# Kernel optimization log

Measured on AMD Instinct MI355X. Metric: run time of the kernel, lower is better.

## Reference

```python
import jax, jax.numpy as jnp
import numpy as np
import math

EMBED_DIM = 1024
MEMORY_DIM = 1024
MEMORY_SIZE = 2048
B, S = 8, 4096


def bitnet_linear(x, W, b):
    """Eval-mode BitNetLinear: 1.58-bit weight quant + 8-bit activation quant."""
    w_scale = jnp.mean(jnp.abs(W))
    qW = jnp.sign(W) * (jnp.abs(W) > 0.5 * w_scale).astype(W.dtype)
    i_scale = jnp.max(jnp.abs(x)) / 127.0
    qx = jnp.clip(jnp.round(x / i_scale), -128.0, 127.0)
    out = jnp.einsum('bsi,oi->bso', qx, qW) * (w_scale * i_scale)
    return out + b


def setup_inputs() -> dict:
    key = jax.random.key(0)
    ks = jax.random.split(key, 9)
    return {
        'x': jax.random.normal(ks[0], (B, S, EMBED_DIM), jnp.float32),
        'memory_keys': jax.random.normal(ks[1], (MEMORY_SIZE, MEMORY_DIM), jnp.float32),
        'memory_values': jax.random.normal(ks[2], (MEMORY_SIZE, EMBED_DIM), jnp.float32),
        'Wk': jax.random.normal(ks[3], (MEMORY_DIM, EMBED_DIM), jnp.float32) * 0.1,
        'bk': jnp.zeros((MEMORY_DIM,), jnp.float32),
        'Wv': jax.random.normal(ks[4], (EMBED_DIM, EMBED_DIM), jnp.float32) * 0.1,
        'bv': jnp.zeros((EMBED_DIM,), jnp.float32),
        'Wo': jax.random.normal(ks[5], (EMBED_DIM, EMBED_DIM), jnp.float32) * 0.1,
        'bo': jnp.zeros((EMBED_DIM,), jnp.float32),
    }


def reference(x, memory_keys, memory_values, Wk, bk, Wv, bv, Wo, bo):
    # quantized key/value projections
    query_keys = bitnet_linear(x, Wk, bk)          # [B, S, Dm]
    _query_values = bitnet_linear(x, Wv, bv)       # computed in original (used only by update path)
    # memory cross-attention over fixed bank
    similarities = jnp.einsum('bsd,md->bsm', query_keys, memory_keys)  # [B, S, M]
    attention_weights = jax.nn.softmax(similarities / math.sqrt(MEMORY_DIM), axis=-1)
    retrieved = jnp.einsum('bsm,me->bse', attention_weights, memory_values)  # [B, S, E]
    output = bitnet_linear(x + retrieved, Wo, bo)
    return output
```

## Files before the change

kernel.cpp:

```cpp
#include <hip/hip_runtime.h>
#include <hip/hip_bf16.h>
#include <stdint.h>
#include <type_traits>

typedef __attribute__((ext_vector_type(8))) short bf16x8;
typedef __attribute__((ext_vector_type(4))) float f32x4;
typedef __attribute__((ext_vector_type(4))) int i32x4;

struct Scalars {
  double sum_wk;
  double sum_wo;
  unsigned int max_x_bits;
  unsigned int max_y_bits;
};

__device__ __forceinline__ unsigned short f2bf(float f) {
  __hip_bfloat16 h = __float2bfloat16(f);
  return *reinterpret_cast<unsigned short*>(&h);
}

__device__ __forceinline__ void async16(void* lds, const void* g) {
  __builtin_amdgcn_global_load_lds((__attribute__((address_space(1))) void*)g,
                                   (__attribute__((address_space(3))) void*)lds, 16, 0, 0);
}

__device__ __forceinline__ void tile_swizzle(int nxShift, int& bx, int& by) {
  const int per = gridDim.x >> 3;
  const int tile = (blockIdx.x & 7) * per + (blockIdx.x >> 3);
  bx = tile & ((1 << nxShift) - 1);
  by = tile >> nxShift;
}

__device__ __forceinline__ f32x4 mm(bf16x8 a, bf16x8 b, f32x4 c) {
  return __builtin_amdgcn_mfma_f32_16x16x32_bf16(a, b, c, 0, 0, 0);
}
__device__ __forceinline__ i32x4 mm(i32x4 a, i32x4 b, i32x4 c) {
  return __builtin_amdgcn_mfma_i32_16x16x64_i8(a, b, c, 0, 0, 0);
}

__global__ __launch_bounds__(256) void abssum_kernel(const float* __restrict__ w, size_t n,
                                                     double* __restrict__ out) {
  size_t tid = (size_t)blockIdx.x * blockDim.x + threadIdx.x;
  size_t stride = (size_t)gridDim.x * blockDim.x;
  double s = 0.0;
  for (size_t i = tid * 4; i < n; i += stride * 4) {
    float4 v = *(const float4*)(w + i);
    s += (double)fabsf(v.x) + (double)fabsf(v.y) + (double)fabsf(v.z) + (double)fabsf(v.w);
  }
#pragma unroll
  for (int o = 32; o > 0; o >>= 1) s += __shfl_xor(s, o);
  __shared__ double sm[4];
  if ((threadIdx.x & 63) == 0) sm[threadIdx.x >> 6] = s;
  __syncthreads();
  if (threadIdx.x == 0) atomicAdd(out, sm[0] + sm[1] + sm[2] + sm[3]);
}

__global__ __launch_bounds__(256) void absmax_kernel(const float* __restrict__ x, size_t n,
                                                     unsigned int* __restrict__ out) {
  size_t tid = (size_t)blockIdx.x * blockDim.x + threadIdx.x;
  size_t stride = (size_t)gridDim.x * blockDim.x;
  float m = 0.0f;
  for (size_t i = tid * 4; i < n; i += stride * 4) {
    float4 v = *(const float4*)(x + i);
    m = fmaxf(m, fmaxf(fmaxf(fabsf(v.x), fabsf(v.y)), fmaxf(fabsf(v.z), fabsf(v.w))));
  }
#pragma unroll
  for (int o = 32; o > 0; o >>= 1) m = fmaxf(m, __shfl_xor(m, o));
  __shared__ float sm[4];
  if ((threadIdx.x & 63) == 0) sm[threadIdx.x >> 6] = m;
  __syncthreads();
  if (threadIdx.x == 0)
    atomicMax(out, __float_as_uint(fmaxf(fmaxf(sm[0], sm[1]), fmaxf(sm[2], sm[3]))));
}

__global__ __launch_bounds__(256) void quant_act_i8_kernel(const float* __restrict__ x,
                                                           char* __restrict__ q,
                                                           const unsigned int* __restrict__ maxbits,
                                                           size_t n) {
  const float isc = __uint_as_float(*maxbits) / 127.0f;
  size_t tid = (size_t)blockIdx.x * blockDim.x + threadIdx.x;
  size_t stride = (size_t)gridDim.x * blockDim.x;
  for (size_t i = tid * 4; i < n; i += stride * 4) {
    float4 v = *(const float4*)(x + i);
    char4 o;
    o.x = (char)(int)fminf(fmaxf(rintf(v.x / isc), -128.f), 127.f);
    o.y = (char)(int)fminf(fmaxf(rintf(v.y / isc), -128.f), 127.f);
    o.z = (char)(int)fminf(fmaxf(rintf(v.z / isc), -128.f), 127.f);
    o.w = (char)(int)fminf(fmaxf(rintf(v.w / isc), -128.f), 127.f);
    *(char4*)(q + i) = o;
  }
}

__global__ __launch_bounds__(256) void quant_w_i8_kernel(const float* __restrict__ W,
                                                         char* __restrict__ qW,
                                                         const double* __restrict__ sum, size_t n) {
  const float wsc = (float)(*sum / (double)n);
  const float thr = 0.5f * wsc;
  size_t tid = (size_t)blockIdx.x * blockDim.x + threadIdx.x;
  size_t stride = (size_t)gridDim.x * blockDim.x;
  for (size_t i = tid * 4; i < n; i += stride * 4) {
    float4 v = *(const float4*)(W + i);
    char4 o;
    o.x = (char)(fabsf(v.x) > thr ? (v.x > 0.f ? 1 : -1) : 0);
    o.y = (char)(fabsf(v.y) > thr ? (v.y > 0.f ? 1 : -1) : 0);
    o.z = (char)(fabsf(v.z) > thr ? (v.z > 0.f ? 1 : -1) : 0);
    o.w = (char)(fabsf(v.w) > thr ? (v.w > 0.f ? 1 : -1) : 0);
    *(char4*)(qW + i) = o;
  }
}

__global__ __launch_bounds__(256) void cast_bf16_kernel(const float* __restrict__ src,
                                                        __hip_bfloat16* __restrict__ dst,
                                                        size_t n) {
  size_t tid = (size_t)blockIdx.x * blockDim.x + threadIdx.x;
  size_t stride = (size_t)gridDim.x * blockDim.x;
  for (size_t i = tid * 4; i < n; i += stride * 4) {
    float4 v = *(const float4*)(src + i);
    ushort4 o;
    o.x = f2bf(v.x); o.y = f2bf(v.y); o.z = f2bf(v.z); o.w = f2bf(v.w);
    *(ushort4*)((unsigned short*)dst + i) = o;
  }
}

__global__ void transpose_mv_kernel(const float* __restrict__ mv,
                                    __hip_bfloat16* __restrict__ mvT) {
  __shared__ float tile[32][33];
  int tx = threadIdx.x, ty = threadIdx.y;
  int e = blockIdx.x * 32 + tx;
  int m = blockIdx.y * 32 + ty;
  tile[ty][tx] = mv[(size_t)m * 1024 + e];
  __syncthreads();
  int om = blockIdx.y * 32 + tx;
  mvT[(size_t)(blockIdx.x * 32 + ty) * 2048 + om] = __float2bfloat16(tile[tx][ty]);
}

__global__ __launch_bounds__(256) void softmax_kernel(__hip_bfloat16* __restrict__ sims) {
  unsigned short* row = (unsigned short*)(sims + (size_t)blockIdx.x * 2048);
  const int t = threadIdx.x;
  const int l = t & 63, wv = t >> 6;
  uint4 r4 = *(const uint4*)(row + t * 8);
  float v[8];
  v[0] = __uint_as_float(r4.x << 16); v[1] = __uint_as_float(r4.x & 0xffff0000u);
  v[2] = __uint_as_float(r4.y << 16); v[3] = __uint_as_float(r4.y & 0xffff0000u);
  v[4] = __uint_as_float(r4.z << 16); v[5] = __uint_as_float(r4.z & 0xffff0000u);
  v[6] = __uint_as_float(r4.w << 16); v[7] = __uint_as_float(r4.w & 0xffff0000u);
  float m = v[0];
#pragma unroll
  for (int i = 1; i < 8; ++i) m = fmaxf(m, v[i]);
#pragma unroll
  for (int o = 32; o > 0; o >>= 1) m = fmaxf(m, __shfl_xor(m, o));
  __shared__ float red[4], red2[4];
  if (l == 0) red[wv] = m;
  __syncthreads();
  m = fmaxf(fmaxf(red[0], red[1]), fmaxf(red[2], red[3]));
  float s = 0.f;
#pragma unroll
  for (int i = 0; i < 8; ++i) { v[i] = expf(v[i] - m); s += v[i]; }
#pragma unroll
  for (int o = 32; o > 0; o >>= 1) s += __shfl_xor(s, o);
  if (l == 0) red2[wv] = s;
  __syncthreads();
  s = red2[0] + red2[1] + red2[2] + red2[3];
  unsigned short b[8];
#pragma unroll
  for (int i = 0; i < 8; ++i) b[i] = f2bf(v[i] / s);
  uint4 o4;
  o4.x = (unsigned)b[0] | ((unsigned)b[1] << 16);
  o4.y = (unsigned)b[2] | ((unsigned)b[3] << 16);
  o4.z = (unsigned)b[4] | ((unsigned)b[5] << 16);
  o4.w = (unsigned)b[6] | ((unsigned)b[7] << 16);
  *(uint4*)(row + t * 8) = o4;
}

#define CFENCE() asm volatile("" ::: "memory")
#define BAR8() { CFENCE(); __builtin_amdgcn_s_barrier(); CFENCE(); }
#define WLGKM(N) { asm volatile("s_waitcnt lgkmcnt(" #N ")" ::: "memory"); __builtin_amdgcn_sched_barrier(0); }
#define WVM(N) asm volatile("s_waitcnt vmcnt(" #N ")" ::: "memory")

template <int EPI>
__global__ __launch_bounds__(512, 2) void gemm8(
    const char* __restrict__ A, const char* __restrict__ B, void* __restrict__ C,
    const float* __restrict__ aux, Scalars* __restrict__ sc,
    int Ndim, int KB, int nxShift) {
  constexpr bool I8 = (EPI >= 3);
  using FR  = typename std::conditional<I8, i32x4, bf16x8>::type;
  using ACC = typename std::conditional<I8, i32x4, f32x4>::type;
  __shared__ __align__(16) char lds[4][2][16384];

  int bx, by;
  tile_swizzle(nxShift, bx, by);
  const int rowBlk = by * 256, colBlk = bx * 256;

  const int t = threadIdx.x, w = t >> 6, l = t & 63;
  const int wm = w >> 2, wn = w & 3;
  const int quad = l >> 4, m16 = l & 15;
  const int NT = KB >> 7, NIT = NT >> 1;

  int voA[2][2], voB[2][2];
#pragma unroll
  for (int hf = 0; hf < 2; ++hf)
#pragma unroll
    for (int j = 0; j < 2; ++j) {
      const int idx = j * 64 + (t >> 3);
      const int kby = ((t & 7) ^ (idx & 7)) << 4;
      voA[hf][j] = (rowBlk + ((idx >> 6) << 7) + (hf << 6) + (idx & 63)) * KB + kby;
      voB[hf][j] = (colBlk + ((idx >> 5) << 6) + (hf << 5) + (idx & 31)) * KB + kby;
    }

  const char* baA[2];
  const char* baB[2];
#pragma unroll
  for (int ks = 0; ks < 2; ++ks) {
    const int x16 = ((ks << 6) + (quad << 4)) ^ ((m16 & 7) << 4);
    baA[ks] = &lds[0][0][(wm * 64 + m16) * 128 + x16];
    baB[ks] = &lds[2][0][(wn * 32 + m16) * 128 + x16];
  }

#define STG_A(slot, hf, tk)                                                         \
  if ((tk) < NT) {                                                                  \
    _Pragma("unroll") for (int j = 0; j < 2; ++j)                                   \
      async16(&lds[hf][slot][j * 8192 + (w << 10)],                                 \
              A + (((size_t)(tk)) << 7) + voA[hf][j]);                              \
  }
#define STG_B(slot, hf, tk)                                                         \
  if ((tk) < NT) {                                                                  \
    _Pragma("unroll") for (int j = 0; j < 2; ++j)                                   \
      async16(&lds[2 + (hf)][slot][j * 8192 + (w << 10)],                           \
              B + (((size_t)(tk)) << 7) + voB[hf][j]);                              \
  }

#define LD_A(dst, slot, hf, f, ks) \
  dst = *(const FR*)(baA[ks] + ((hf)*32768 + (slot)*16384 + (f)*2048));
#define LD_B(dst, slot, hf, gg, ks) \
  dst = *(const FR*)(baB[ks] + ((hf)*32768 + (slot)*16384 + (gg)*2048));

#define R_A0(s) { _Pragma("unroll") for (int f_ = 0; f_ < 4; ++f_) { LD_A(af[f_][0], s, 0, f_, 0); LD_A(af[f_][1], s, 0, f_, 1); } }
#define R_A1(s) { _Pragma("unroll") for (int f_ = 0; f_ < 4; ++f_) { LD_A(af[f_][0], s, 1, f_, 0); LD_A(af[f_][1], s, 1, f_, 1); } }
#define R_B0(s) { _Pragma("unroll") for (int g_ = 0; g_ < 2; ++g_) { LD_B(b0[g_][0], s, 0, g_, 0); LD_B(b0[g_][1], s, 0, g_, 1); } }
#define R_B1(s) { _Pragma("unroll") for (int g_ = 0; g_ < 2; ++g_) { LD_B(b1[g_][0], s, 1, g_, 0); LD_B(b1[g_][1], s, 1, g_, 1); } }

#define MM8(FO, GO, BR)                                                             \
  __builtin_amdgcn_s_setprio(1);                                                    \
  _Pragma("unroll") for (int f_ = 0; f_ < 4; ++f_)                                  \
    _Pragma("unroll") for (int g_ = 0; g_ < 2; ++g_) {                              \
      acc[(FO) + f_][(GO) + g_] = mm(af[f_][0], BR[g_][0], acc[(FO) + f_][(GO) + g_]); \
      acc[(FO) + f_][(GO) + g_] = mm(af[f_][1], BR[g_][1], acc[(FO) + f_][(GO) + g_]); \
    }                                                                               \
  __builtin_amdgcn_s_setprio(0);

#define TSTEP(s, tk, last)                                                          \
  {                                                                                 \
                     \
    R_B1(s);                                                                        \
    STG_A((s) ^ 1, 1, (tk) + 1);                                                    \
    BAR8(); WLGKM(4);                                                               \
    MM8(0, 0, b0);                                                                  \
    BAR8();                                                                         \
        \
    STG_A(s, 0, (tk) + 2);                                                          \
    BAR8(); WLGKM(0);                                                               \
    MM8(0, 2, b1);                                                                  \
    R_A1(s);                                                                        \
    BAR8();                                                                         \
                                                                \
    STG_B(s, 0, (tk) + 2);                                                          \
    BAR8(); WLGKM(0);                                                               \
    MM8(4, 0, b0);                                                                  \
    BAR8();                                                                         \
           \
    STG_B(s, 1, (tk) + 2);                                                          \
    if (last) { WVM(0); } else { WVM(6); }                                          \
    BAR8();                                                                         \
    MM8(4, 2, b1);                                                                  \
    R_A0((s) ^ 1);                                                                  \
    R_B0((s) ^ 1);                                                                  \
    BAR8();                                                                         \
  }

  FR af[4][2], b0[2][2], b1[2][2];
  ACC acc[8][4] = {};

  STG_A(0, 0, 0); STG_B(0, 0, 0); STG_B(0, 1, 0); STG_A(0, 1, 0);
  CFENCE();
  STG_A(1, 0, 1); STG_B(1, 0, 1); STG_B(1, 1, 1);
  WVM(6);
  BAR8();
  R_A0(0); R_B0(0);

  for (int it = 0; it < NIT; ++it) {
    const bool last = (it == NIT - 1);
    TSTEP(0, it * 2, last);
    TSTEP(1, it * 2 + 1, last);
  }

  float sK = 0.0f;
  if constexpr (EPI == 3)
    sK = (float)(sc->sum_wk * (1.0 / 1048576.0)) * (__uint_as_float(sc->max_x_bits) / 127.0f);
  if constexpr (EPI == 4)
    sK = (float)(sc->sum_wo * (1.0 / 1048576.0)) * (__uint_as_float(sc->max_y_bits) / 127.0f);

  float amax = 0.0f;
#pragma unroll
  for (int f = 0; f < 8; ++f) {
#pragma unroll
    for (int g = 0; g < 4; ++g) {
      const int col = colBlk + wn * 64 + g * 16 + m16;
#pragma unroll
      for (int rg = 0; rg < 4; ++rg) {
        const int row = rowBlk + wm * 128 + f * 16 + quad * 4 + rg;
        if constexpr (EPI == 1) {
          ((__hip_bfloat16*)C)[(size_t)row * Ndim + col] =
              __float2bfloat16(acc[f][g][rg] * 0.03125f);
        } else if constexpr (EPI == 2) {
          float v = acc[f][g][rg] + aux[(size_t)row * Ndim + col];
          ((float*)C)[(size_t)row * Ndim + col] = v;
          amax = fmaxf(amax, fabsf(v));
        } else if constexpr (EPI == 3) {
          ((__hip_bfloat16*)C)[(size_t)row * Ndim + col] =
              __float2bfloat16((float)acc[f][g][rg] * sK + aux[col]);
        } else {
          ((float*)C)[(size_t)row * Ndim + col] = (float)acc[f][g][rg] * sK + aux[col];
        }
      }
    }
  }

  if constexpr (EPI == 2) {
    __shared__ float wred[8];
#pragma unroll
    for (int o = 32; o > 0; o >>= 1) amax = fmaxf(amax, __shfl_xor(amax, o));
    if (l == 0) wred[w] = amax;
    __syncthreads();
    if (t == 0) {
      float m = wred[0];
#pragma unroll
      for (int i = 1; i < 8; ++i) m = fmaxf(m, wred[i]);
      atomicMax(&sc->max_y_bits, __float_as_uint(m));
    }
  }
#undef STG_A
#undef STG_B
#undef LD_A
#undef LD_B
#undef R_A0
#undef R_A1
#undef R_B0
#undef R_B1
#undef MM8
#undef TSTEP
}

extern "C" void kernel_launch(void* const* d_in, const int* in_sizes, int n_in,
                              void* d_out, int out_size, void* d_ws, size_t ws_size,
                              hipStream_t stream) {
  (void)in_sizes; (void)n_in; (void)out_size; (void)ws_size;
  const float* x  = (const float*)d_in[0];
  const float* mk = (const float*)d_in[1];
  const float* mv = (const float*)d_in[2];
  const float* Wk = (const float*)d_in[3];
  const float* bk = (const float*)d_in[4];
  const float* Wo = (const float*)d_in[7];
  const float* bo = (const float*)d_in[8];
  float* out = (float*)d_out;

  const int M = 32768, E = 1024, MEM = 2048;

  char* ws = (char*)d_ws;
  Scalars* sc = (Scalars*)ws;
  const size_t off0 = 256;
  char* qx8 = ws + off0;
  __hip_bfloat16* qk = (__hip_bfloat16*)(ws + off0 + (size_t)M * E);
  float* y = (float*)(ws + off0);
  const size_t off1 = off0 + (size_t)M * E * 4;
  __hip_bfloat16* sims = (__hip_bfloat16*)(ws + off1);
  char* qy8 = (char*)sims;
  const size_t off2 = off1 + (size_t)M * MEM * 2;
  char* qWk8 = ws + off2;
  char* qWo8 = qWk8 + (size_t)E * E;
  __hip_bfloat16* mkb = (__hip_bfloat16*)(qWo8 + (size_t)E * E);
  __hip_bfloat16* mvT = mkb + (size_t)MEM * E;

  hipMemsetAsync(ws, 0, 256, stream);

  abssum_kernel<<<dim3(256), dim3(256), 0, stream>>>(Wk, (size_t)E * E, &sc->sum_wk);
  abssum_kernel<<<dim3(256), dim3(256), 0, stream>>>(Wo, (size_t)E * E, &sc->sum_wo);
  absmax_kernel<<<dim3(2048), dim3(256), 0, stream>>>(x, (size_t)M * E, &sc->max_x_bits);

  quant_act_i8_kernel<<<dim3(2048), dim3(256), 0, stream>>>(x, qx8, &sc->max_x_bits, (size_t)M * E);
  quant_w_i8_kernel<<<dim3(256), dim3(256), 0, stream>>>(Wk, qWk8, &sc->sum_wk, (size_t)E * E);
  quant_w_i8_kernel<<<dim3(256), dim3(256), 0, stream>>>(Wo, qWo8, &sc->sum_wo, (size_t)E * E);
  cast_bf16_kernel<<<dim3(256), dim3(256), 0, stream>>>(mk, mkb, (size_t)MEM * E);
  transpose_mv_kernel<<<dim3(E / 32, MEM / 32), dim3(32, 32), 0, stream>>>(mv, mvT);

  gemm8<3><<<dim3((E / 256) * (M / 256)), dim3(512), 0, stream>>>(
      qx8, qWk8, qk, bk, sc, E, E, 2);
  gemm8<1><<<dim3((MEM / 256) * (M / 256)), dim3(512), 0, stream>>>(
      (const char*)qk, (const char*)mkb, sims, nullptr, sc, MEM, 2 * E, 3);
  softmax_kernel<<<dim3(M), dim3(256), 0, stream>>>(sims);
  gemm8<2><<<dim3((E / 256) * (M / 256)), dim3(512), 0, stream>>>(
      (const char*)sims, (const char*)mvT, y, x, sc, E, 2 * MEM, 2);
  quant_act_i8_kernel<<<dim3(2048), dim3(256), 0, stream>>>(y, qy8, &sc->max_y_bits, (size_t)M * E);
  gemm8<4><<<dim3((E / 256) * (M / 256)), dim3(512), 0, stream>>>(
      qy8, qWo8, out, bo, sc, E, E, 2);
}
```

Before: 774.4 us.

## Switch GEMMs to 32x32 MFMA and merge prep kernels into two launches

Replaces the 16x16 MFMA tiles in the templated GEMM with 32x32x16 bf16 and 32x32x32 i8 MFMAs, which changes the LDS fragment addressing, swizzle offsets and epilogue row mapping. It also fuses the abssum and absmax reductions into one stats kernel and the weight quantisation, bf16 cast, transpose and activation quantisation into one prep kernel. The aim is fewer LDS reads per MFMA, higher matrix throughput and less launch overhead. The trailing barrier in the pipeline step is removed, which risks LDS races, and the new lane mapping risks correctness errors.

```diff
diff --git a/kernel.cpp b/kernel.cpp
--- a/kernel.cpp
+++ b/kernel.cpp
@@ -4,8 +4,9 @@
 #include <type_traits>
 
 typedef __attribute__((ext_vector_type(8))) short bf16x8;
-typedef __attribute__((ext_vector_type(4))) float f32x4;
 typedef __attribute__((ext_vector_type(4))) int i32x4;
+typedef __attribute__((ext_vector_type(16))) float f32x16;
+typedef __attribute__((ext_vector_type(16))) int i32x16;
 
 struct Scalars {
   double sum_wk;
@@ -31,46 +32,112 @@
   by = tile >> nxShift;
 }
 
-__device__ __forceinline__ f32x4 mm(bf16x8 a, bf16x8 b, f32x4 c) {
-  return __builtin_amdgcn_mfma_f32_16x16x32_bf16(a, b, c, 0, 0, 0);
-}
-__device__ __forceinline__ i32x4 mm(i32x4 a, i32x4 b, i32x4 c) {
-  return __builtin_amdgcn_mfma_i32_16x16x64_i8(a, b, c, 0, 0, 0);
-}
-
-__global__ __launch_bounds__(256) void abssum_kernel(const float* __restrict__ w, size_t n,
-                                                     double* __restrict__ out) {
-  size_t tid = (size_t)blockIdx.x * blockDim.x + threadIdx.x;
-  size_t stride = (size_t)gridDim.x * blockDim.x;
-  double s = 0.0;
-  for (size_t i = tid * 4; i < n; i += stride * 4) {
-    float4 v = *(const float4*)(w + i);
-    s += (double)fabsf(v.x) + (double)fabsf(v.y) + (double)fabsf(v.z) + (double)fabsf(v.w);
-  }
-#pragma unroll
-  for (int o = 32; o > 0; o >>= 1) s += __shfl_xor(s, o);
-  __shared__ double sm[4];
-  if ((threadIdx.x & 63) == 0) sm[threadIdx.x >> 6] = s;
-  __syncthreads();
-  if (threadIdx.x == 0) atomicAdd(out, sm[0] + sm[1] + sm[2] + sm[3]);
-}
-
-__global__ __launch_bounds__(256) void absmax_kernel(const float* __restrict__ x, size_t n,
-                                                     unsigned int* __restrict__ out) {
-  size_t tid = (size_t)blockIdx.x * blockDim.x + threadIdx.x;
-  size_t stride = (size_t)gridDim.x * blockDim.x;
-  float m = 0.0f;
-  for (size_t i = tid * 4; i < n; i += stride * 4) {
-    float4 v = *(const float4*)(x + i);
-    m = fmaxf(m, fmaxf(fmaxf(fabsf(v.x), fabsf(v.y)), fmaxf(fabsf(v.z), fabsf(v.w))));
-  }
-#pragma unroll
-  for (int o = 32; o > 0; o >>= 1) m = fmaxf(m, __shfl_xor(m, o));
-  __shared__ float sm[4];
-  if ((threadIdx.x & 63) == 0) sm[threadIdx.x >> 6] = m;
-  __syncthreads();
-  if (threadIdx.x == 0)
-    atomicMax(out, __float_as_uint(fmaxf(fmaxf(sm[0], sm[1]), fmaxf(sm[2], sm[3]))));
+__device__ __forceinline__ f32x16 mm32(bf16x8 a, bf16x8 b, f32x16 c) {
+  return __builtin_amdgcn_mfma_f32_32x32x16_bf16(a, b, c, 0, 0, 0);
+}
+__device__ __forceinline__ i32x16 mm32(i32x4 a, i32x4 b, i32x16 c) {
+  return __builtin_amdgcn_mfma_i32_32x32x32_i8(a, b, c, 0, 0, 0);
+}
+
+__global__ __launch_bounds__(256) void stats_kernel(const float* __restrict__ Wk,
+                                                    const float* __restrict__ Wo,
+                                                    const float* __restrict__ x,
+                                                    Scalars* __restrict__ sc) {
+  const int which = blockIdx.y;
+  size_t tid = (size_t)blockIdx.x * 256 + threadIdx.x;
+  size_t stride = (size_t)gridDim.x * 256;
+  if (which < 2) {
+    const float* w = which ? Wo : Wk;
+    const size_t n = 1048576;
+    double s = 0.0;
+    for (size_t i = tid * 4; i < n; i += stride * 4) {
+      float4 v = *(const float4*)(w + i);
+      s += (double)fabsf(v.x) + (double)fabsf(v.y) + (double)fabsf(v.z) + (double)fabsf(v.w);
+    }
+#pragma unroll
+    for (int o = 32; o > 0; o >>= 1) s += __shfl_xor(s, o);
+    __shared__ double sm[4];
+    if ((threadIdx.x & 63) == 0) sm[threadIdx.x >> 6] = s;
+    __syncthreads();
+    if (threadIdx.x == 0)
+      atomicAdd(which ? &sc->sum_wo : &sc->sum_wk, sm[0] + sm[1] + sm[2] + sm[3]);
+  } else {
+    const size_t n = (size_t)32768 * 1024;
+    float m = 0.0f;
+    for (size_t i = tid * 4; i < n; i += stride * 4) {
+      float4 v = *(const float4*)(x + i);
+      m = fmaxf(m, fmaxf(fmaxf(fabsf(v.x), fabsf(v.y)), fmaxf(fabsf(v.z), fabsf(v.w))));
+    }
+#pragma unroll
+    for (int o = 32; o > 0; o >>= 1) m = fmaxf(m, __shfl_xor(m, o));
+    __shared__ float smf[4];
+    if ((threadIdx.x & 63) == 0) smf[threadIdx.x >> 6] = m;
+    __syncthreads();
+    if (threadIdx.x == 0)
+      atomicMax(&sc->max_x_bits,
+                __float_as_uint(fmaxf(fmaxf(smf[0], smf[1]), fmaxf(smf[2], smf[3]))));
+  }
+}
+
+__global__ __launch_bounds__(256) void prep_kernel(
+    const float* __restrict__ Wk, const float* __restrict__ Wo,
+    const float* __restrict__ mk, const float* __restrict__ mv,
+    const float* __restrict__ x, char* __restrict__ qWk8, char* __restrict__ qWo8,
+    __hip_bfloat16* __restrict__ mkb, __hip_bfloat16* __restrict__ mvT,
+    char* __restrict__ qx8, const Scalars* __restrict__ sc) {
+  __shared__ float tl[32][33];
+  const int which = blockIdx.y;
+  const int t = threadIdx.x;
+  size_t tid = (size_t)blockIdx.x * 256 + t;
+  size_t stride = (size_t)gridDim.x * 256;
+  if (which < 2) {
+    const float* W = which ? Wo : Wk;
+    char* q = which ? qWo8 : qWk8;
+    const double sum = which ? sc->sum_wo : sc->sum_wk;
+    const float thr = 0.5f * (float)(sum * (1.0 / 1048576.0));
+    const size_t n = 1048576;
+    for (size_t i = tid * 4; i < n; i += stride * 4) {
+      float4 v = *(const float4*)(W + i);
+      char4 o;
+      o.x = (char)(fabsf(v.x) > thr ? (v.x > 0.f ? 1 : -1) : 0);
+      o.y = (char)(fabsf(v.y) > thr ? (v.y > 0.f ? 1 : -1) : 0);
+      o.z = (char)(fabsf(v.z) > thr ? (v.z > 0.f ? 1 : -1) : 0);
+      o.w = (char)(fabsf(v.w) > thr ? (v.w > 0.f ? 1 : -1) : 0);
+      *(char4*)(q + i) = o;
+    }
+  } else if (which == 2) {
+    const size_t n = (size_t)2048 * 1024;
+    for (size_t i = tid * 4; i < n; i += stride * 4) {
+      float4 v = *(const float4*)(mk + i);
+      ushort4 o;
+      o.x = f2bf(v.x); o.y = f2bf(v.y); o.z = f2bf(v.z); o.w = f2bf(v.w);
+      *(ushort4*)((unsigned short*)mkb + i) = o;
+    }
+  } else if (which == 3) {
+    const int ti = blockIdx.x & 31;
+    const int tj = blockIdx.x >> 5;
+    const int tx = t & 31, ty = t >> 5;
+#pragma unroll
+    for (int r = 0; r < 4; ++r)
+      tl[ty + r * 8][tx] = mv[(size_t)(tj * 32 + ty + r * 8) * 1024 + ti * 32 + tx];
+    __syncthreads();
+#pragma unroll
+    for (int r = 0; r < 4; ++r)
+      mvT[(size_t)(ti * 32 + ty + r * 8) * 2048 + tj * 32 + tx] =
+          __float2bfloat16(tl[tx][ty + r * 8]);
+  } else {
+    const float isc = __uint_as_float(sc->max_x_bits) / 127.0f;
+    const size_t n = (size_t)32768 * 1024;
+    for (size_t i = tid * 4; i < n; i += stride * 4) {
+      float4 v = *(const float4*)(x + i);
+      char4 o;
+      o.x = (char)(int)fminf(fmaxf(rintf(v.x / isc), -128.f), 127.f);
+      o.y = (char)(int)fminf(fmaxf(rintf(v.y / isc), -128.f), 127.f);
+      o.z = (char)(int)fminf(fmaxf(rintf(v.z / isc), -128.f), 127.f);
+      o.w = (char)(int)fminf(fmaxf(rintf(v.w / isc), -128.f), 127.f);
+      *(char4*)(qx8 + i) = o;
+    }
+  }
 }
 
 __global__ __launch_bounds__(256) void quant_act_i8_kernel(const float* __restrict__ x,
@@ -91,49 +158,6 @@
   }
 }
 
-__global__ __launch_bounds__(256) void quant_w_i8_kernel(const float* __restrict__ W,
-                                                         char* __restrict__ qW,
-                                                         const double* __restrict__ sum, size_t n) {
-  const float wsc = (float)(*sum / (double)n);
-  const float thr = 0.5f * wsc;
-  size_t tid = (size_t)blockIdx.x * blockDim.x + threadIdx.x;
-  size_t stride = (size_t)gridDim.x * blockDim.x;
-  for (size_t i = tid * 4; i < n; i += stride * 4) {
-    float4 v = *(const float4*)(W + i);
-    char4 o;
-    o.x = (char)(fabsf(v.x) > thr ? (v.x > 0.f ? 1 : -1) : 0);
-    o.y = (char)(fabsf(v.y) > thr ? (v.y > 0.f ? 1 : -1) : 0);
-    o.z = (char)(fabsf(v.z) > thr ? (v.z > 0.f ? 1 : -1) : 0);
-    o.w = (char)(fabsf(v.w) > thr ? (v.w > 0.f ? 1 : -1) : 0);
-    *(char4*)(qW + i) = o;
-  }
-}
-
-__global__ __launch_bounds__(256) void cast_bf16_kernel(const float* __restrict__ src,
-                                                        __hip_bfloat16* __restrict__ dst,
-                                                        size_t n) {
-  size_t tid = (size_t)blockIdx.x * blockDim.x + threadIdx.x;
-  size_t stride = (size_t)gridDim.x * blockDim.x;
-  for (size_t i = tid * 4; i < n; i += stride * 4) {
-    float4 v = *(const float4*)(src + i);
-    ushort4 o;
-    o.x = f2bf(v.x); o.y = f2bf(v.y); o.z = f2bf(v.z); o.w = f2bf(v.w);
-    *(ushort4*)((unsigned short*)dst + i) = o;
-  }
-}
-
-__global__ void transpose_mv_kernel(const float* __restrict__ mv,
-                                    __hip_bfloat16* __restrict__ mvT) {
-  __shared__ float tile[32][33];
-  int tx = threadIdx.x, ty = threadIdx.y;
-  int e = blockIdx.x * 32 + tx;
-  int m = blockIdx.y * 32 + ty;
-  tile[ty][tx] = mv[(size_t)m * 1024 + e];
-  __syncthreads();
-  int om = blockIdx.y * 32 + tx;
-  mvT[(size_t)(blockIdx.x * 32 + ty) * 2048 + om] = __float2bfloat16(tile[tx][ty]);
-}
-
 __global__ __launch_bounds__(256) void softmax_kernel(__hip_bfloat16* __restrict__ sims) {
   unsigned short* row = (unsigned short*)(sims + (size_t)blockIdx.x * 2048);
   const int t = threadIdx.x;
@@ -184,7 +208,7 @@
     int Ndim, int KB, int nxShift) {
   constexpr bool I8 = (EPI >= 3);
   using FR  = typename std::conditional<I8, i32x4, bf16x8>::type;
-  using ACC = typename std::conditional<I8, i32x4, f32x4>::type;
+  using ACC = typename std::conditional<I8, i32x16, f32x16>::type;
   __shared__ __align__(16) char lds[4][2][16384];
 
   int bx, by;
@@ -193,7 +217,7 @@
 
   const int t = threadIdx.x, w = t >> 6, l = t & 63;
   const int wm = w >> 2, wn = w & 3;
-  const int quad = l >> 4, m16 = l & 15;
+  const int l31 = l & 31, hi = l >> 5;
   const int NT = KB >> 7, NIT = NT >> 1;
 
   int voA[2][2], voB[2][2];
@@ -207,14 +231,12 @@
       voB[hf][j] = (colBlk + ((idx >> 5) << 6) + (hf << 5) + (idx & 31)) * KB + kby;
     }
 
-  const char* baA[2];
-  const char* baB[2];
-#pragma unroll
-  for (int ks = 0; ks < 2; ++ks) {
-    const int x16 = ((ks << 6) + (quad << 4)) ^ ((m16 & 7) << 4);
-    baA[ks] = &lds[0][0][(wm * 64 + m16) * 128 + x16];
-    baB[ks] = &lds[2][0][(wn * 32 + m16) * 128 + x16];
-  }
+  int ofsK[4];
+#pragma unroll
+  for (int ks = 0; ks < 4; ++ks)
+    ofsK[ks] = ((((ks ^ ((l >> 1) & 3)) << 1) | (hi ^ (l & 1))) << 4);
+  const char* bA = &lds[0][0][0] + (wm * 64 + l31) * 128;
+  const char* bB = &lds[2][0][0] + (wn * 32 + l31) * 128;
 
 #define STG_A(slot, hf, tk)                                                         \
   if ((tk) < NT) {                                                                  \
@@ -229,23 +251,21 @@
               B + (((size_t)(tk)) << 7) + voB[hf][j]);                              \
   }
 
-#define LD_A(dst, slot, hf, f, ks) \
-  dst = *(const FR*)(baA[ks] + ((hf)*32768 + (slot)*16384 + (f)*2048));
-#define LD_B(dst, slot, hf, gg, ks) \
-  dst = *(const FR*)(baB[ks] + ((hf)*32768 + (slot)*16384 + (gg)*2048));
-
-#define R_A0(s) { _Pragma("unroll") for (int f_ = 0; f_ < 4; ++f_) { LD_A(af[f_][0], s, 0, f_, 0); LD_A(af[f_][1], s, 0, f_, 1); } }
-#define R_A1(s) { _Pragma("unroll") for (int f_ = 0; f_ < 4; ++f_) { LD_A(af[f_][0], s, 1, f_, 0); LD_A(af[f_][1], s, 1, f_, 1); } }
-#define R_B0(s) { _Pragma("unroll") for (int g_ = 0; g_ < 2; ++g_) { LD_B(b0[g_][0], s, 0, g_, 0); LD_B(b0[g_][1], s, 0, g_, 1); } }
-#define R_B1(s) { _Pragma("unroll") for (int g_ = 0; g_ < 2; ++g_) { LD_B(b1[g_][0], s, 1, g_, 0); LD_B(b1[g_][1], s, 1, g_, 1); } }
-
-#define MM8(FO, GO, BR)                                                             \
+#define LD_A(dst, slot, hf, f01, ks) \
+  dst = *(const FR*)(bA + ((hf) * 32768 + (slot) * 16384 + (f01) * 4096) + ofsK[ks]);
+#define LD_B(dst, slot, nh, ks) \
+  dst = *(const FR*)(bB + ((nh) * 32768 + (slot) * 16384) + ofsK[ks]);
+
+#define R_A0(s) { _Pragma("unroll") for (int f_ = 0; f_ < 2; ++f_) _Pragma("unroll") for (int k_ = 0; k_ < 4; ++k_) LD_A(af[f_][k_], s, 0, f_, k_); }
+#define R_A1(s) { _Pragma("unroll") for (int f_ = 0; f_ < 2; ++f_) _Pragma("unroll") for (int k_ = 0; k_ < 4; ++k_) LD_A(af[f_][k_], s, 1, f_, k_); }
+#define R_B0(s) { _Pragma("unroll") for (int k_ = 0; k_ < 4; ++k_) LD_B(b0[k_], s, 0, k_); }
+#define R_B1(s) { _Pragma("unroll") for (int k_ = 0; k_ < 4; ++k_) LD_B(b1[k_], s, 1, k_); }
+
+#define MM32(MH, NH, BR)                                                            \
   __builtin_amdgcn_s_setprio(1);                                                    \
-  _Pragma("unroll") for (int f_ = 0; f_ < 4; ++f_)                                  \
-    _Pragma("unroll") for (int g_ = 0; g_ < 2; ++g_) {                              \
-      acc[(FO) + f_][(GO) + g_] = mm(af[f_][0], BR[g_][0], acc[(FO) + f_][(GO) + g_]); \
-      acc[(FO) + f_][(GO) + g_] = mm(af[f_][1], BR[g_][1], acc[(FO) + f_][(GO) + g_]); \
-    }                                                                               \
+  _Pragma("unroll") for (int k_ = 0; k_ < 4; ++k_)                                  \
+    _Pragma("unroll") for (int f_ = 0; f_ < 2; ++f_)                                \
+      acc[(MH) * 2 + f_][NH] = mm32(af[f_][k_], BR[k_], acc[(MH) * 2 + f_][NH]);    \
   __builtin_amdgcn_s_setprio(0);
 
 #define TSTEP(s, tk, last)                                                          \
@@ -254,31 +274,29 @@
     R_B1(s);                                                                        \
     STG_A((s) ^ 1, 1, (tk) + 1);                                                    \
     BAR8(); WLGKM(4);                                                               \
-    MM8(0, 0, b0);                                                                  \
+    MM32(0, 0, b0);                                                                 \
     BAR8();                                                                         \
         \
     STG_A(s, 0, (tk) + 2);                                                          \
     BAR8(); WLGKM(0);                                                               \
-    MM8(0, 2, b1);                                                                  \
+    MM32(0, 1, b1);                                                                 \
     R_A1(s);                                                                        \
     BAR8();                                                                         \
                                                                 \
     STG_B(s, 0, (tk) + 2);                                                          \
     BAR8(); WLGKM(0);                                                               \
-    MM8(4, 0, b0);                                                                  \
+    MM32(1, 0, b0);                                                                 \
     BAR8();                                                                         \
            \
     STG_B(s, 1, (tk) + 2);                                                          \
     if (last) { WVM(0); } else { WVM(6); }                                          \
     BAR8();                                                                         \
-    MM8(4, 2, b1);                                                                  \
-    R_A0((s) ^ 1);                                                                  \
-    R_B0((s) ^ 1);                                                                  \
-    BAR8();                                                                         \
-  }
-
-  FR af[4][2], b0[2][2], b1[2][2];
-  ACC acc[8][4] = {};
+    MM32(1, 1, b1);                                                                 \
+    R_A0((s) ^ 1); R_B0((s) ^ 1);                                                   \
+  }
+
+  FR af[2][4], b0[4], b1[4];
+  ACC acc[4][2] = {};
 
   STG_A(0, 0, 0); STG_B(0, 0, 0); STG_B(0, 1, 0); STG_A(0, 1, 0);
   CFENCE();
@@ -301,25 +319,25 @@
 
   float amax = 0.0f;
 #pragma unroll
-  for (int f = 0; f < 8; ++f) {
-#pragma unroll
-    for (int g = 0; g < 4; ++g) {
-      const int col = colBlk + wn * 64 + g * 16 + m16;
-#pragma unroll
-      for (int rg = 0; rg < 4; ++rg) {
-        const int row = rowBlk + wm * 128 + f * 16 + quad * 4 + rg;
+  for (int f = 0; f < 4; ++f) {
+#pragma unroll
+    for (int g = 0; g < 2; ++g) {
+      const int col = colBlk + wn * 64 + g * 32 + l31;
+#pragma unroll
+      for (int r = 0; r < 16; ++r) {
+        const int row = rowBlk + wm * 128 + f * 32 + (r & 3) + 8 * (r >> 2) + 4 * hi;
         if constexpr (EPI == 1) {
           ((__hip_bfloat16*)C)[(size_t)row * Ndim + col] =
-              __float2bfloat16(acc[f][g][rg] * 0.03125f);
+              __float2bfloat16(acc[f][g][r] * 0.03125f);
         } else if constexpr (EPI == 2) {
-          float v = acc[f][g][rg] + aux[(size_t)row * Ndim + col];
+          float v = acc[f][g][r] + aux[(size_t)row * Ndim + col];
           ((float*)C)[(size_t)row * Ndim + col] = v;
           amax = fmaxf(amax, fabsf(v));
         } else if constexpr (EPI == 3) {
           ((__hip_bfloat16*)C)[(size_t)row * Ndim + col] =
-              __float2bfloat16((float)acc[f][g][rg] * sK + aux[col]);
+              __float2bfloat16((float)acc[f][g][r] * sK + aux[col]);
         } else {
-          ((float*)C)[(size_t)row * Ndim + col] = (float)acc[f][g][rg] * sK + aux[col];
+          ((float*)C)[(size_t)row * Ndim + col] = (float)acc[f][g][r] * sK + aux[col];
         }
       }
     }
@@ -346,7 +364,7 @@
 #undef R_A1
 #undef R_B0
 #undef R_B1
-#undef MM8
+#undef MM32
 #undef TSTEP
 }
 
@@ -382,15 +400,9 @@
 
   hipMemsetAsync(ws, 0, 256, stream);
 
-  abssum_kernel<<<dim3(256), dim3(256), 0, stream>>>(Wk, (size_t)E * E, &sc->sum_wk);
-  abssum_kernel<<<dim3(256), dim3(256), 0, stream>>>(Wo, (size_t)E * E, &sc->sum_wo);
-  absmax_kernel<<<dim3(2048), dim3(256), 0, stream>>>(x, (size_t)M * E, &sc->max_x_bits);
-
-  quant_act_i8_kernel<<<dim3(2048), dim3(256), 0, stream>>>(x, qx8, &sc->max_x_bits, (size_t)M * E);
-  quant_w_i8_kernel<<<dim3(256), dim3(256), 0, stream>>>(Wk, qWk8, &sc->sum_wk, (size_t)E * E);
-  quant_w_i8_kernel<<<dim3(256), dim3(256), 0, stream>>>(Wo, qWo8, &sc->sum_wo, (size_t)E * E);
-  cast_bf16_kernel<<<dim3(256), dim3(256), 0, stream>>>(mk, mkb, (size_t)MEM * E);
-  transpose_mv_kernel<<<dim3(E / 32, MEM / 32), dim3(32, 32), 0, stream>>>(mv, mvT);
+  stats_kernel<<<dim3(1024, 3), dim3(256), 0, stream>>>(Wk, Wo, x, sc);
+  prep_kernel<<<dim3(2048, 5), dim3(256), 0, stream>>>(Wk, Wo, mk, mv, x, qWk8, qWo8,
+                                                       mkb, mvT, qx8, sc);
 
   gemm8<3><<<dim3((E / 256) * (M / 256)), dim3(512), 0, stream>>>(
       qx8, qWk8, qk, bk, sc, E, E, 2);
```

After: 738.0 us. 1.05x faster.
